# Kernel tuning notes

Measured on AMD Instinct MI355X. Metric: run time of the kernel, lower is better.

The kernel has to match this reference:

```python
import jax, jax.numpy as jnp
import numpy as np

B, L, E, H = 512, 100, 256, 256
T = 100          # max_length (== sourceL for TSP)
C_EXPLORE = 10.0  # tanh_exploration
N_GLIMPSES = 1


def setup_inputs() -> dict:
    key = jax.random.key(0)
    ks = jax.random.split(key, 19)
    s = 0.05
    f = lambda k, shape: jax.random.normal(k, shape, dtype=jnp.float32) * s
    return dict(
        decoder_input=f(ks[0], (B, E)),
        embedded_inputs=f(ks[1], (L, B, E)),
        h0=f(ks[2], (B, H)), c0=f(ks[3], (B, H)),
        context=f(ks[4], (L, B, H)),
        Wi=f(ks[5], (4 * H, E)), bi=f(ks[6], (4 * H,)),
        Wh=f(ks[7], (4 * H, H)), bh=f(ks[8], (4 * H,)),
        g_Wq=f(ks[9], (H, H)), g_bq=f(ks[10], (H,)),
        g_Wref=f(ks[11], (H, H)), g_bref=f(ks[12], (H,)),
        g_v=f(ks[13], (H,)),
        p_Wq=f(ks[14], (H, H)), p_bq=f(ks[15], (H,)),
        p_Wref=f(ks[16], (H, H)), p_bref=f(ks[17], (H,)),
        p_v=f(ks[18], (H,)),
    )


def _decode(decoder_input, embedded_inputs, h0, c0, context,
            Wi, bi, Wh, bh,
            g_Wq, g_bq, g_Wref, g_bref, g_v,
            p_Wq, p_bq, p_Wref, p_bref, p_v):
    # Conv1d(dim, dim, 1) over context == feature matmul; context is static,
    # so project refs once (same math as per-step projection in torch code).
    ctx = jnp.transpose(context, (1, 2, 0))                       # [B,H,L]
    e_g = jnp.einsum('oh,bhl->bol', g_Wref, ctx) + g_bref[None, :, None]
    e_p = jnp.einsum('oh,bhl->bol', p_Wref, ctx) + p_bref[None, :, None]
    rows = jnp.arange(B)

    def attn_logits(q, e, Wq, bq, v):
        qp = q @ Wq.T + bq                                        # [B,H]
        return jnp.einsum('h,bhl->bl', v, jnp.tanh(qp[:, :, None] + e))

    def apply_mask(step, logits, mask, prev):
        # step 0: mask position 0; step 1: unmask 0, mask prev; step>1: mask prev
        m1 = jnp.where(step == 1, mask.at[:, 0].set(False), mask)
        m1 = m1.at[rows, prev].set(True)
        m0 = mask.at[:, 0].set(True)
        new_mask = jnp.where(step == 0, m0, m1)
        return jnp.where(new_mask, -jnp.inf, logits), new_mask

    def step_fn(carry, step):
        x, hx, cx, mask, prev = carry
        gates = x @ Wi.T + bi + hx @ Wh.T + bh                    # [B,4H]
        ig, fg, cg, og = jnp.split(gates, 4, axis=1)
        cy = jax.nn.sigmoid(fg) * cx + jax.nn.sigmoid(ig) * jnp.tanh(cg)
        hy = jax.nn.sigmoid(og) * jnp.tanh(cy)
        g_l = hy
        for _ in range(N_GLIMPSES):
            lg = attn_logits(g_l, e_g, g_Wq, g_bq, g_v)
            lg, mask = apply_mask(step, lg, mask, prev)
            g_l = jnp.einsum('bhl,bl->bh', e_g, jax.nn.softmax(lg, axis=1))
        lp = attn_logits(g_l, e_p, p_Wq, p_bq, p_v)
        lp = C_EXPLORE * jnp.tanh(lp)                             # use_tanh=True
        lp, mask = apply_mask(step, lp, mask, prev)
        probs = jax.nn.softmax(lp, axis=1)                        # [B,L]
        idxs = jnp.argmax(probs, axis=1)                          # greedy
        sels = embedded_inputs[idxs, rows, :]                     # [B,E]
        return (sels, hy, cy, mask, idxs), (probs, idxs)

    mask0 = jnp.zeros((B, L), dtype=bool)
    prev0 = jnp.zeros((B,), dtype=jnp.int32)
    carry0 = (decoder_input, h0, c0, mask0, prev0)
    (xT, hx, cx, maskT, prevT), (probs_seq, sel_seq) = jax.lax.scan(
        step_fn, carry0, jnp.arange(T))
    return probs_seq, sel_seq, hx, cx


def reference(decoder_input, embedded_inputs, h0, c0, context,
              Wi, bi, Wh, bh,
              g_Wq, g_bq, g_Wref, g_bref, g_v,
              p_Wq, p_bq, p_Wref, p_bref, p_v):
    return _decode(decoder_input, embedded_inputs, h0, c0, context,
                   Wi, bi, Wh, bh,
                   g_Wq, g_bq, g_Wref, g_bref, g_v,
                   p_Wq, p_bq, p_Wref, p_bref, p_v)
```

## Files before the change

### kernel.cpp

```cpp
#include <hip/hip_runtime.h>
#include <math.h>

namespace {

constexpr int Bn = 512;
constexpr int Ln = 100;
constexpr int En = 256;
constexpr int Hn = 256;
constexpr int Tn = 100;

__device__ __forceinline__ float fast_tanh(float x) {
  float ax = fabsf(x);
  float e = __expf(-2.0f * ax);
  float t = (1.0f - e) / (1.0f + e);
  return copysignf(t, x);
}
__device__ __forceinline__ float fast_sigm(float x) {
  return 1.0f / (1.0f + __expf(-x));
}

__device__ __forceinline__ float wave_max(float v) {
#pragma unroll
  for (int off = 32; off > 0; off >>= 1) v = fmaxf(v, __shfl_xor(v, off, 64));
  return v;
}
__device__ __forceinline__ float wave_sum(float v) {
#pragma unroll
  for (int off = 32; off > 0; off >>= 1) v += __shfl_xor(v, off, 64);
  return v;
}

__global__ void init_kernel(const float* __restrict__ dec, const float* __restrict__ h0,
                            const float* __restrict__ c0, float* __restrict__ x,
                            float* __restrict__ h, float* __restrict__ c,
                            int* __restrict__ mask, int* __restrict__ prev) {
  int i = blockIdx.x * 256 + threadIdx.x;
  if (i < Bn * En) x[i] = dec[i];
  if (i < Bn * Hn) { h[i] = h0[i]; c[i] = c0[i]; }
  if (i < Bn * Ln) mask[i] = 0;
  if (i < Bn) prev[i] = 0;
}

__global__ void transpose256_kernel(const float* __restrict__ W, float* __restrict__ WT) {
  int h = blockIdx.x, k = threadIdx.x;
  WT[k * 256 + h] = W[h * 256 + k];
}

__global__ __launch_bounds__(256) void precompute_e_kernel(
    const float* __restrict__ WT, const float* __restrict__ bref,
    const float* __restrict__ context, float* __restrict__ e_t) {
  int b = blockIdx.x;
  int l0 = blockIdx.y * 25;
  int h = threadIdx.x;
  __shared__ float ctx_s[25][256];
  for (int li = 0; li < 25; ++li)
    ctx_s[li][h] = context[((size_t)(l0 + li) * Bn + b) * Hn + h];
  __syncthreads();
  float acc[25];
  float bias = bref[h];
#pragma unroll
  for (int li = 0; li < 25; ++li) acc[li] = bias;
  for (int k = 0; k < 256; ++k) {
    float w = WT[k * 256 + h];
#pragma unroll
    for (int li = 0; li < 25; ++li) acc[li] += w * ctx_s[li][k];
  }
#pragma unroll
  for (int li = 0; li < 25; ++li)
    e_t[((size_t)b * Ln + (l0 + li)) * Hn + h] = acc[li];
}

__global__ __launch_bounds__(256) void lstm_kernel(
    const float* __restrict__ x, const float* __restrict__ h_in,
    const float* __restrict__ c_in, const float* __restrict__ Wi,
    const float* __restrict__ Wh, const float* __restrict__ bi,
    const float* __restrict__ bh, float* __restrict__ h_out,
    float* __restrict__ c_out) {
  const int b0 = blockIdx.x * 32;
  const int n0 = blockIdx.y * 16;
  const int tid = threadIdx.x;
  const int n = tid & 15;
  const int br = tid >> 4;
  __shared__ float A_s[32][33];
  __shared__ float W_s[4][16][33];
  float acc[4][2];
  const int nn = n0 + n;
#pragma unroll
  for (int g = 0; g < 4; ++g) {
    float bias = bi[g * 256 + nn] + bh[g * 256 + nn];
    acc[g][0] = bias;
    acc[g][1] = bias;
  }
  const int bb = tid >> 3, q = tid & 7;
  for (int k0 = 0; k0 < 512; k0 += 32) {
    const float* Asrc = (k0 < 256) ? x : h_in;
    const float* Wsrc = (k0 < 256) ? Wi : Wh;
    const int kb = k0 & 255;
    __syncthreads();
    float4 av = *(const float4*)(Asrc + (b0 + bb) * 256 + kb + q * 4);
    A_s[q * 4 + 0][bb] = av.x;
    A_s[q * 4 + 1][bb] = av.y;
    A_s[q * 4 + 2][bb] = av.z;
    A_s[q * 4 + 3][bb] = av.w;
#pragma unroll
    for (int s = 0; s < 2; ++s) {
      int sl = tid + s * 256;
      int g = sl >> 7;
      int nl = (sl >> 3) & 15;
      int qq = sl & 7;
      float4 wv = *(const float4*)(Wsrc + ((g * 256 + n0 + nl) * 256) + kb + qq * 4);
      W_s[g][nl][qq * 4 + 0] = wv.x;
      W_s[g][nl][qq * 4 + 1] = wv.y;
      W_s[g][nl][qq * 4 + 2] = wv.z;
      W_s[g][nl][qq * 4 + 3] = wv.w;
    }
    __syncthreads();
#pragma unroll
    for (int kk = 0; kk < 32; ++kk) {
      float a0 = A_s[kk][2 * br];
      float a1 = A_s[kk][2 * br + 1];
#pragma unroll
      for (int g = 0; g < 4; ++g) {
        float w = W_s[g][n][kk];
        acc[g][0] += a0 * w;
        acc[g][1] += a1 * w;
      }
    }
  }
#pragma unroll
  for (int m = 0; m < 2; ++m) {
    int b = b0 + 2 * br + m;
    float ig = acc[0][m], fg = acc[1][m], cg = acc[2][m], og = acc[3][m];
    float cold = c_in[b * 256 + nn];
    float cy = fast_sigm(fg) * cold + fast_sigm(ig) * fast_tanh(cg);
    float hy = fast_sigm(og) * fast_tanh(cy);
    c_out[b * 256 + nn] = cy;
    h_out[b * 256 + nn] = hy;
  }
}

__global__ __launch_bounds__(256) void qp_gemm_kernel(
    const float* __restrict__ A, const float* __restrict__ Wq,
    const float* __restrict__ bq, float* __restrict__ C) {
  const int b0 = blockIdx.x * 32;
  const int n0 = blockIdx.y * 16;
  const int tid = threadIdx.x;
  const int n = tid & 15;
  const int br = tid >> 4;
  __shared__ float A_s[32][33];
  __shared__ float W_s[16][33];
  float bias = bq[n0 + n];
  float acc0 = bias, acc1 = bias;
  const int bb = tid >> 3, q = tid & 7;
  for (int k0 = 0; k0 < 256; k0 += 32) {
    __syncthreads();
    float4 av = *(const float4*)(A + (b0 + bb) * 256 + k0 + q * 4);
    A_s[q * 4 + 0][bb] = av.x;
    A_s[q * 4 + 1][bb] = av.y;
    A_s[q * 4 + 2][bb] = av.z;
    A_s[q * 4 + 3][bb] = av.w;
    if (tid < 128) {
      int nl = tid >> 3, qq = tid & 7;
      float4 wv = *(const float4*)(Wq + (n0 + nl) * 256 + k0 + qq * 4);
      W_s[nl][qq * 4 + 0] = wv.x;
      W_s[nl][qq * 4 + 1] = wv.y;
      W_s[nl][qq * 4 + 2] = wv.z;
      W_s[nl][qq * 4 + 3] = wv.w;
    }
    __syncthreads();
#pragma unroll
    for (int kk = 0; kk < 32; ++kk) {
      float a0 = A_s[kk][2 * br];
      float a1 = A_s[kk][2 * br + 1];
      float w = W_s[n][kk];
      acc0 += a0 * w;
      acc1 += a1 * w;
    }
  }
  C[(b0 + 2 * br) * 256 + n0 + n] = acc0;
  C[(b0 + 2 * br + 1) * 256 + n0 + n] = acc1;
}

__global__ __launch_bounds__(256) void glimpse_kernel(
    const float* __restrict__ qp, const float* __restrict__ v,
    const float* __restrict__ e_t, int* __restrict__ mask,
    const int* __restrict__ prev, float* __restrict__ gl, int step) {
  const int tid = threadIdx.x;
  const int b = blockIdx.x;
  const int li = tid & 127;
  const int half = tid >> 7;
  __shared__ float qp_s[256], v_s[256];
  __shared__ float logit_s[128];
  __shared__ float p_s[128];
  __shared__ float wred_m[2], wred_s[2];
  qp_s[tid] = qp[b * 256 + tid];
  v_s[tid] = v[tid];
  __syncthreads();
  float part = 0.0f;
  if (li < Ln) {
    const float4* ep = (const float4*)(e_t + ((size_t)b * Ln + li) * Hn + half * 128);
    const float4* qp4 = (const float4*)(qp_s + half * 128);
    const float4* v4 = (const float4*)(v_s + half * 128);
#pragma unroll 8
    for (int j = 0; j < 32; ++j) {
      float4 ev = ep[j];
      float4 qv = qp4[j];
      float4 vv = v4[j];
      part += vv.x * fast_tanh(qv.x + ev.x);
      part += vv.y * fast_tanh(qv.y + ev.y);
      part += vv.z * fast_tanh(qv.z + ev.z);
      part += vv.w * fast_tanh(qv.w + ev.w);
    }
  }
  if (half == 1) logit_s[li] = part;
  __syncthreads();
  float lgv = -INFINITY;
  if (half == 0 && li < Ln) {
    float a = part + logit_s[li];
    int pb = prev[b];
    int m = mask[b * Ln + li];
    if (step == 0) {
      if (li == 0) m = 1;
    } else {
      if (step == 1 && li == 0) m = 0;
      if (li == pb) m = 1;
    }
    mask[b * Ln + li] = m;
    lgv = m ? -INFINITY : a;
  }
  float wm = wave_max((tid < 128) ? lgv : -INFINITY);
  if (tid < 128 && (tid & 63) == 0) wred_m[tid >> 6] = wm;
  __syncthreads();
  float mx = fmaxf(wred_m[0], wred_m[1]);
  float pvv = (lgv == -INFINITY) ? 0.0f : __expf(lgv - mx);
  float wsm = wave_sum((tid < 128) ? pvv : 0.0f);
  if (tid < 128 && (tid & 63) == 0) wred_s[tid >> 6] = wsm;
  __syncthreads();
  float tot = wred_s[0] + wred_s[1];
  if (tid < 128) p_s[li] = pvv / tot;
  __syncthreads();
  {
    const int h = tid;
    const float* eb = e_t + (size_t)b * Ln * Hn + h;
    float a = 0.0f;
#pragma unroll 4
    for (int l = 0; l < Ln; ++l) a += eb[(size_t)l * Hn] * p_s[l];
    gl[b * Hn + h] = a;
  }
}

__global__ __launch_bounds__(256) void pointer_kernel(
    const float* __restrict__ qp, const float* __restrict__ v,
    const float* __restrict__ e_t, const int* __restrict__ mask,
    int* __restrict__ prev, const float* __restrict__ emb,
    float* __restrict__ xout, float* __restrict__ out, int step) {
  const int tid = threadIdx.x;
  const int b = blockIdx.x;
  const int li = tid & 127;
  const int half = tid >> 7;
  __shared__ float qp_s[256], v_s[256];
  __shared__ float logit_s[128];
  __shared__ float wred_m[2], wred_s[2];
  __shared__ float wval[2];
  __shared__ int widx[2];
  __shared__ int sel_s;
  qp_s[tid] = qp[b * 256 + tid];
  v_s[tid] = v[tid];
  __syncthreads();
  float part = 0.0f;
  if (li < Ln) {
    const float4* ep = (const float4*)(e_t + ((size_t)b * Ln + li) * Hn + half * 128);
    const float4* qp4 = (const float4*)(qp_s + half * 128);
    const float4* v4 = (const float4*)(v_s + half * 128);
#pragma unroll 8
    for (int j = 0; j < 32; ++j) {
      float4 ev = ep[j];
      float4 qv = qp4[j];
      float4 vv = v4[j];
      part += vv.x * fast_tanh(qv.x + ev.x);
      part += vv.y * fast_tanh(qv.y + ev.y);
      part += vv.z * fast_tanh(qv.z + ev.z);
      part += vv.w * fast_tanh(qv.w + ev.w);
    }
  }
  if (half == 1) logit_s[li] = part;
  __syncthreads();
  float lgv = -INFINITY;
  if (half == 0 && li < Ln) {
    float a = part + logit_s[li];
    float lp = 10.0f * fast_tanh(a);
    int m = mask[b * Ln + li];
    lgv = m ? -INFINITY : lp;
  }
  float wm = wave_max((tid < 128) ? lgv : -INFINITY);
  if (tid < 128 && (tid & 63) == 0) wred_m[tid >> 6] = wm;
  __syncthreads();
  float mx = fmaxf(wred_m[0], wred_m[1]);
  float pvv = (lgv == -INFINITY) ? 0.0f : __expf(lgv - mx);
  float wsm = wave_sum((tid < 128) ? pvv : 0.0f);
  if (tid < 128 && (tid & 63) == 0) wred_s[tid >> 6] = wsm;
  __syncthreads();
  float tot = wred_s[0] + wred_s[1];
  float p = pvv / tot;
  if (half == 0 && li < Ln) out[((size_t)step * Bn + b) * Ln + li] = p;
  float val = (tid < 128 && li < Ln) ? p : -1.0f;
  int idx = li;
#pragma unroll
  for (int off = 32; off > 0; off >>= 1) {
    float ov = __shfl_down(val, off, 64);
    int oi = __shfl_down(idx, off, 64);
    if (ov > val || (ov == val && oi < idx)) { val = ov; idx = oi; }
  }
  if (tid < 128 && (tid & 63) == 0) { wval[tid >> 6] = val; widx[tid >> 6] = idx; }
  __syncthreads();
  if (tid == 0) {
    int sel = (wval[1] > wval[0] || (wval[1] == wval[0] && widx[1] < widx[0]))
                  ? widx[1] : widx[0];
    sel_s = sel;
    prev[b] = sel;
    out[(size_t)Tn * Bn * Ln + (size_t)step * Bn + b] = (float)sel;
  }
  __syncthreads();
  int sel = sel_s;
  xout[b * En + tid] = emb[((size_t)sel * Bn + b) * En + tid];
}

__global__ void finalize_kernel(const float* __restrict__ h,
                                const float* __restrict__ c,
                                float* __restrict__ out) {
  int i = blockIdx.x * 256 + threadIdx.x;
  const size_t base = (size_t)Tn * Bn * Ln + (size_t)Tn * Bn;
  if (i < Bn * Hn) {
    out[base + i] = h[i];
    out[base + (size_t)Bn * Hn + i] = c[i];
  }
}

}

extern "C" void kernel_launch(void* const* d_in, const int* in_sizes, int n_in,
                              void* d_out, int out_size, void* d_ws, size_t ws_size,
                              hipStream_t stream) {
  (void)in_sizes; (void)n_in; (void)out_size; (void)ws_size;
  const float* dec   = (const float*)d_in[0];
  const float* emb   = (const float*)d_in[1];
  const float* h0    = (const float*)d_in[2];
  const float* c0    = (const float*)d_in[3];
  const float* ctx   = (const float*)d_in[4];
  const float* Wi    = (const float*)d_in[5];
  const float* bi    = (const float*)d_in[6];
  const float* Wh    = (const float*)d_in[7];
  const float* bh    = (const float*)d_in[8];
  const float* gWq   = (const float*)d_in[9];
  const float* gbq   = (const float*)d_in[10];
  const float* gWref = (const float*)d_in[11];
  const float* gbref = (const float*)d_in[12];
  const float* gv    = (const float*)d_in[13];
  const float* pWq   = (const float*)d_in[14];
  const float* pbq   = (const float*)d_in[15];
  const float* pWref = (const float*)d_in[16];
  const float* pbref = (const float*)d_in[17];
  const float* pv    = (const float*)d_in[18];

  float* ws = (float*)d_ws;
  float* e_g   = ws;  ws += (size_t)Bn * Hn * Ln;
  float* e_p   = ws;  ws += (size_t)Bn * Hn * Ln;
  float* WTg   = ws;  ws += 256 * 256;
  float* WTp   = ws;  ws += 256 * 256;
  float* xbuf  = ws;  ws += Bn * En;
  float* hbuf  = ws;  ws += 2 * Bn * Hn;
  float* cbuf  = ws;  ws += 2 * Bn * Hn;
  float* qpg   = ws;  ws += Bn * Hn;
  float* qpp   = ws;  ws += Bn * Hn;
  float* glbuf = ws;  ws += Bn * Hn;
  int* maskb   = (int*)ws;  ws += Bn * Ln;
  int* prevb   = (int*)ws;  ws += Bn;
  float* out = (float*)d_out;

  init_kernel<<<512, 256, 0, stream>>>(dec, h0, c0, xbuf, hbuf, cbuf, maskb, prevb);
  transpose256_kernel<<<256, 256, 0, stream>>>(gWref, WTg);
  transpose256_kernel<<<256, 256, 0, stream>>>(pWref, WTp);
  precompute_e_kernel<<<dim3(512, 4), 256, 0, stream>>>(WTg, gbref, ctx, e_g);
  precompute_e_kernel<<<dim3(512, 4), 256, 0, stream>>>(WTp, pbref, ctx, e_p);

  for (int t = 0; t < Tn; ++t) {
    const float* hin = hbuf + (t & 1) * Bn * Hn;
    float* hout      = hbuf + ((t + 1) & 1) * Bn * Hn;
    const float* cin = cbuf + (t & 1) * Bn * Hn;
    float* cout      = cbuf + ((t + 1) & 1) * Bn * Hn;
    lstm_kernel<<<dim3(16, 16), 256, 0, stream>>>(xbuf, hin, cin, Wi, Wh, bi, bh, hout, cout);
    qp_gemm_kernel<<<dim3(16, 16), 256, 0, stream>>>(hout, gWq, gbq, qpg);
    glimpse_kernel<<<512, 256, 0, stream>>>(qpg, gv, e_g, maskb, prevb, glbuf, t);
    qp_gemm_kernel<<<dim3(16, 16), 256, 0, stream>>>(glbuf, pWq, pbq, qpp);
    pointer_kernel<<<512, 256, 0, stream>>>(qpp, pv, e_p, maskb, prevb, emb, xbuf, out, t);
  }
  finalize_kernel<<<512, 256, 0, stream>>>(hbuf, cbuf, out);
}
```

Before: 9.481 ms.

## Fold pointer query projection into precomputed context and fuse glimpse with pointer

Because the glimpse is a softmax-weighted sum of e_g, its projection by pWq equals a weighted sum over a precomputed f_p = (pWq·gWref)·ctx + pWq·gbref. This drops the per-step glimpse-to-query GEMM and fuses the glimpse and pointer kernels into one launch per step, which also keeps the mask in a register. In exchange it adds a third B×L×H precomputed buffer and three setup kernels, and each step now reads an extra B×L×H tensor f_p.

```diff
diff --git a/kernel.cpp b/kernel.cpp
--- a/kernel.cpp
+++ b/kernel.cpp
@@ -44,6 +44,27 @@
 __global__ void transpose256_kernel(const float* __restrict__ W, float* __restrict__ WT) {
   int h = blockIdx.x, k = threadIdx.x;
   WT[k * 256 + h] = W[h * 256 + k];
+}
+
+__global__ void matmul_M_kernel(const float* __restrict__ pWq,
+                                const float* __restrict__ gWref,
+                                float* __restrict__ M) {
+  int i = blockIdx.x, j = threadIdx.x;
+  float acc = 0.0f;
+  for (int h = 0; h < 256; ++h) acc += pWq[i * 256 + h] * gWref[h * 256 + j];
+  M[i * 256 + j] = acc;
+}
+
+__global__ void mb_kernel(const float* __restrict__ pWq,
+                          const float* __restrict__ gbref,
+                          float* __restrict__ mb) {
+  __shared__ float gb[256];
+  int i = threadIdx.x;
+  gb[i] = gbref[i];
+  __syncthreads();
+  float acc = 0.0f;
+  for (int h = 0; h < 256; ++h) acc += pWq[i * 256 + h] * gb[h];
+  mb[i] = acc;
 }
 
 __global__ __launch_bounds__(256) void precompute_e_kernel(
@@ -181,30 +202,36 @@
   C[(b0 + 2 * br + 1) * 256 + n0 + n] = acc1;
 }
 
-__global__ __launch_bounds__(256) void glimpse_kernel(
-    const float* __restrict__ qp, const float* __restrict__ v,
-    const float* __restrict__ e_t, int* __restrict__ mask,
-    const int* __restrict__ prev, float* __restrict__ gl, int step) {
+__global__ __launch_bounds__(256) void attn_fused_kernel(
+    const float* __restrict__ qp_g, const float* __restrict__ gv,
+    const float* __restrict__ pv, const float* __restrict__ pbq,
+    const float* __restrict__ e_g, const float* __restrict__ f_p,
+    const float* __restrict__ e_p, int* __restrict__ mask,
+    int* __restrict__ prev, const float* __restrict__ emb,
+    float* __restrict__ xout, float* __restrict__ out, int step) {
   const int tid = threadIdx.x;
   const int b = blockIdx.x;
   const int li = tid & 127;
   const int half = tid >> 7;
-  __shared__ float qp_s[256], v_s[256];
-  __shared__ float logit_s[128];
-  __shared__ float p_s[128];
+  __shared__ float q1_s[256], vg_s[256], vp_s[256], q2_s[256];
+  __shared__ float logit_s[128], p_s[128];
   __shared__ float wred_m[2], wred_s[2];
-  qp_s[tid] = qp[b * 256 + tid];
-  v_s[tid] = v[tid];
+  __shared__ float wval[2];
+  __shared__ int widx[2];
+  __shared__ int sel_s;
+  q1_s[tid] = qp_g[b * 256 + tid];
+  vg_s[tid] = gv[tid];
+  vp_s[tid] = pv[tid];
   __syncthreads();
   float part = 0.0f;
   if (li < Ln) {
-    const float4* ep = (const float4*)(e_t + ((size_t)b * Ln + li) * Hn + half * 128);
-    const float4* qp4 = (const float4*)(qp_s + half * 128);
-    const float4* v4 = (const float4*)(v_s + half * 128);
+    const float4* ep = (const float4*)(e_g + ((size_t)b * Ln + li) * Hn + half * 128);
+    const float4* q4 = (const float4*)(q1_s + half * 128);
+    const float4* v4 = (const float4*)(vg_s + half * 128);
 #pragma unroll 8
     for (int j = 0; j < 32; ++j) {
       float4 ev = ep[j];
-      float4 qv = qp4[j];
+      float4 qv = q4[j];
       float4 vv = v4[j];
       part += vv.x * fast_tanh(qv.x + ev.x);
       part += vv.y * fast_tanh(qv.y + ev.y);
@@ -215,6 +242,7 @@
   if (half == 1) logit_s[li] = part;
   __syncthreads();
   float lgv = -INFINITY;
+  int mreg = 1;
   if (half == 0 && li < Ln) {
     float a = part + logit_s[li];
     int pb = prev[b];
@@ -226,6 +254,7 @@
       if (li == pb) m = 1;
     }
     mask[b * Ln + li] = m;
+    mreg = m;
     lgv = m ? -INFINITY : a;
   }
   float wm = wave_max((tid < 128) ? lgv : -INFINITY);
@@ -240,42 +269,22 @@
   if (tid < 128) p_s[li] = pvv / tot;
   __syncthreads();
   {
-    const int h = tid;
-    const float* eb = e_t + (size_t)b * Ln * Hn + h;
-    float a = 0.0f;
+    float acc = pbq[tid];
+    const float* fb = f_p + (size_t)b * Ln * Hn + tid;
 #pragma unroll 4
-    for (int l = 0; l < Ln; ++l) a += eb[(size_t)l * Hn] * p_s[l];
-    gl[b * Hn + h] = a;
-  }
-}
-
-__global__ __launch_bounds__(256) void pointer_kernel(
-    const float* __restrict__ qp, const float* __restrict__ v,
-    const float* __restrict__ e_t, const int* __restrict__ mask,
-    int* __restrict__ prev, const float* __restrict__ emb,
-    float* __restrict__ xout, float* __restrict__ out, int step) {
-  const int tid = threadIdx.x;
-  const int b = blockIdx.x;
-  const int li = tid & 127;
-  const int half = tid >> 7;
-  __shared__ float qp_s[256], v_s[256];
-  __shared__ float logit_s[128];
-  __shared__ float wred_m[2], wred_s[2];
-  __shared__ float wval[2];
-  __shared__ int widx[2];
-  __shared__ int sel_s;
-  qp_s[tid] = qp[b * 256 + tid];
-  v_s[tid] = v[tid];
-  __syncthreads();
-  float part = 0.0f;
+    for (int l = 0; l < Ln; ++l) acc += p_s[l] * fb[(size_t)l * Hn];
+    q2_s[tid] = acc;
+  }
+  __syncthreads();
+  part = 0.0f;
   if (li < Ln) {
-    const float4* ep = (const float4*)(e_t + ((size_t)b * Ln + li) * Hn + half * 128);
-    const float4* qp4 = (const float4*)(qp_s + half * 128);
-    const float4* v4 = (const float4*)(v_s + half * 128);
+    const float4* ep = (const float4*)(e_p + ((size_t)b * Ln + li) * Hn + half * 128);
+    const float4* q4 = (const float4*)(q2_s + half * 128);
+    const float4* v4 = (const float4*)(vp_s + half * 128);
 #pragma unroll 8
     for (int j = 0; j < 32; ++j) {
       float4 ev = ep[j];
-      float4 qv = qp4[j];
+      float4 qv = q4[j];
       float4 vv = v4[j];
       part += vv.x * fast_tanh(qv.x + ev.x);
       part += vv.y * fast_tanh(qv.y + ev.y);
@@ -285,22 +294,21 @@
   }
   if (half == 1) logit_s[li] = part;
   __syncthreads();
-  float lgv = -INFINITY;
+  lgv = -INFINITY;
   if (half == 0 && li < Ln) {
     float a = part + logit_s[li];
     float lp = 10.0f * fast_tanh(a);
-    int m = mask[b * Ln + li];
-    lgv = m ? -INFINITY : lp;
-  }
-  float wm = wave_max((tid < 128) ? lgv : -INFINITY);
+    lgv = mreg ? -INFINITY : lp;
+  }
+  wm = wave_max((tid < 128) ? lgv : -INFINITY);
   if (tid < 128 && (tid & 63) == 0) wred_m[tid >> 6] = wm;
   __syncthreads();
-  float mx = fmaxf(wred_m[0], wred_m[1]);
-  float pvv = (lgv == -INFINITY) ? 0.0f : __expf(lgv - mx);
-  float wsm = wave_sum((tid < 128) ? pvv : 0.0f);
+  mx = fmaxf(wred_m[0], wred_m[1]);
+  pvv = (lgv == -INFINITY) ? 0.0f : __expf(lgv - mx);
+  wsm = wave_sum((tid < 128) ? pvv : 0.0f);
   if (tid < 128 && (tid & 63) == 0) wred_s[tid >> 6] = wsm;
   __syncthreads();
-  float tot = wred_s[0] + wred_s[1];
+  tot = wred_s[0] + wred_s[1];
   float p = pvv / tot;
   if (half == 0 && li < Ln) out[((size_t)step * Bn + b) * Ln + li] = p;
   float val = (tid < 128 && li < Ln) ? p : -1.0f;
@@ -365,14 +373,16 @@
   float* ws = (float*)d_ws;
   float* e_g   = ws;  ws += (size_t)Bn * Hn * Ln;
   float* e_p   = ws;  ws += (size_t)Bn * Hn * Ln;
+  float* f_p   = ws;  ws += (size_t)Bn * Hn * Ln;
   float* WTg   = ws;  ws += 256 * 256;
   float* WTp   = ws;  ws += 256 * 256;
+  float* Mbuf  = ws;  ws += 256 * 256;
+  float* MT    = ws;  ws += 256 * 256;
+  float* mb    = ws;  ws += 256;
   float* xbuf  = ws;  ws += Bn * En;
   float* hbuf  = ws;  ws += 2 * Bn * Hn;
   float* cbuf  = ws;  ws += 2 * Bn * Hn;
   float* qpg   = ws;  ws += Bn * Hn;
-  float* qpp   = ws;  ws += Bn * Hn;
-  float* glbuf = ws;  ws += Bn * Hn;
   int* maskb   = (int*)ws;  ws += Bn * Ln;
   int* prevb   = (int*)ws;  ws += Bn;
   float* out = (float*)d_out;
@@ -380,8 +390,12 @@
   init_kernel<<<512, 256, 0, stream>>>(dec, h0, c0, xbuf, hbuf, cbuf, maskb, prevb);
   transpose256_kernel<<<256, 256, 0, stream>>>(gWref, WTg);
   transpose256_kernel<<<256, 256, 0, stream>>>(pWref, WTp);
+  matmul_M_kernel<<<256, 256, 0, stream>>>(pWq, gWref, Mbuf);
+  mb_kernel<<<1, 256, 0, stream>>>(pWq, gbref, mb);
+  transpose256_kernel<<<256, 256, 0, stream>>>(Mbuf, MT);
   precompute_e_kernel<<<dim3(512, 4), 256, 0, stream>>>(WTg, gbref, ctx, e_g);
   precompute_e_kernel<<<dim3(512, 4), 256, 0, stream>>>(WTp, pbref, ctx, e_p);
+  precompute_e_kernel<<<dim3(512, 4), 256, 0, stream>>>(MT, mb, ctx, f_p);
 
   for (int t = 0; t < Tn; ++t) {
     const float* hin = hbuf + (t & 1) * Bn * Hn;
@@ -390,9 +404,8 @@
     float* cout      = cbuf + ((t + 1) & 1) * Bn * Hn;
     lstm_kernel<<<dim3(16, 16), 256, 0, stream>>>(xbuf, hin, cin, Wi, Wh, bi, bh, hout, cout);
     qp_gemm_kernel<<<dim3(16, 16), 256, 0, stream>>>(hout, gWq, gbq, qpg);
-    glimpse_kernel<<<512, 256, 0, stream>>>(qpg, gv, e_g, maskb, prevb, glbuf, t);
-    qp_gemm_kernel<<<dim3(16, 16), 256, 0, stream>>>(glbuf, pWq, pbq, qpp);
-    pointer_kernel<<<512, 256, 0, stream>>>(qpp, pv, e_p, maskb, prevb, emb, xbuf, out, t);
+    attn_fused_kernel<<<512, 256, 0, stream>>>(qpg, gv, pv, pbq, e_g, f_p, e_p,
+                                               maskb, prevb, emb, xbuf, out, t);
   }
   finalize_kernel<<<512, 256, 0, stream>>>(hbuf, cbuf, out);
 }
```

After: 8.001 ms. 15.6% less time.
